# Kernel tuning notes

Hardware: AMD Instinct MI355X
Metric: run time of the kernel (lower is better)

## Reference

```python
import jax, jax.numpy as jnp
import numpy as np

B, T, EMB, NDIM = 8, 2048, 1024, 1024


def setup_inputs() -> dict:
    key = jax.random.key(0)
    k1, k2, k3, k4 = jax.random.split(key, 4)
    X = jax.random.normal(k1, (B, T, EMB), dtype=jnp.float32)
    # Linear(emb, ndim, bias=False); stored as [emb, ndim] so projection is X @ W.
    scale = 1.0 / np.sqrt(EMB)
    Wq = jax.random.normal(k2, (EMB, NDIM), dtype=jnp.float32) * scale
    Wk = jax.random.normal(k3, (EMB, NDIM), dtype=jnp.float32) * scale
    Wv = jax.random.normal(k4, (EMB, NDIM), dtype=jnp.float32) * scale
    return {"X": X, "Wq": Wq, "Wk": Wk, "Wv": Wv}


def reference(X, Wq, Wk, Wv):
    ndim = Wq.shape[-1]
    T_ = X.shape[1]
    Q = X @ Wq  # [B,T,ndim]
    K = X @ Wk  # [B,T,ndim]
    V = X @ Wv  # [B,T,ndim]
    # scores[b,t,s] = Q[b,t] . K[b,s], scaled by ndim^-0.5
    scores = jnp.einsum("btd,bsd->bts", Q, K) * (ndim ** -0.5)
    mask = jnp.tril(jnp.ones((T_, T_), dtype=bool))  # causal lower-triangular
    scores = jnp.where(mask, scores, -jnp.inf)
    # NOTE: source uses F.softmax(..., dim=1) -> normalize over the QUERY axis
    # (columns of the [T,T] matrix), not the usual key axis. Replicated faithfully.
    probs = jax.nn.softmax(scores, axis=1)
    # dropout is identity in eval / p=0 deterministic baseline
    return probs @ V  # [B,T,ndim]
```

## Files before the change

kernel.cpp:

```cpp
#include <hip/hip_runtime.h>
#include <hip/hip_bf16.h>

#define B_   8
#define T_   2048
#define EMB_ 1024
#define ND_  1024
#define NTB2 8

typedef __attribute__((ext_vector_type(8))) short   bf8_t;
typedef __attribute__((ext_vector_type(4))) float   f32x4;

__device__ __forceinline__ unsigned short f2bf(float f) {
  union { float f; unsigned int u; } c; c.f = f;
  unsigned int u = c.u;
  unsigned int r = (u + 0x7FFFu + ((u >> 16) & 1u)) >> 16;
  return (unsigned short)r;
}

__device__ __forceinline__ float bf2f(unsigned short b) {
  union { unsigned int u; float f; } c; c.u = ((unsigned int)b) << 16;
  return c.f;
}

__device__ __forceinline__ void gload_lds16(const unsigned short* g, unsigned short* l) {
  __builtin_amdgcn_global_load_lds(
      (const __attribute__((address_space(1))) unsigned int*)g,
      (__attribute__((address_space(3))) unsigned int*)l,
      16, 0, 0);
}

#define SB0() __builtin_amdgcn_sched_barrier(0)
#define BAR() __builtin_amdgcn_s_barrier()

__device__ __forceinline__ void stage_half(const unsigned short* __restrict__ g, int lda,
                                           unsigned short* lhalf, int wave, int lane) {
  const int r3 = lane >> 3, c3 = lane & 7;
  const int colsw = ((c3 ^ r3) << 3);
#pragma unroll
  for (int j = 0; j < 2; ++j) {
    const int row = wave * 8 + r3 + 64 * j;
    gload_lds16(g + (size_t)row * lda + colsw, lhalf + wave * 512 + j * 4096);
  }
}

__device__ __forceinline__ bf8_t read_frag(const unsigned short* half, int r, int ks, int lane) {
  const int col = (((ks) << 5) + ((lane >> 4) << 3)) ^ ((r & 7) << 3);
  return *(const bf8_t*)(half + r * 64 + col);
}

__device__ __forceinline__ int swz_ep(int x) { return ((x >> 1) & 7) << 4; }

__global__ void __launch_bounds__(256) cvt_x_kernel(const float* __restrict__ in,
                                                    unsigned short* __restrict__ out) {
  const int i = (blockIdx.x * 256 + threadIdx.x) * 4;
  float4 v = *(const float4*)(in + i);
  ushort4 o = make_ushort4(f2bf(v.x), f2bf(v.y), f2bf(v.z), f2bf(v.w));
  *(ushort4*)(out + i) = o;
}

__global__ void __launch_bounds__(256) transpose_w_kernel(const float* __restrict__ W,
                                                          unsigned short* __restrict__ Wt,
                                                          float cscale) {
  __shared__ unsigned short tile[32][33];
  const int n0 = blockIdx.x * 32, k0 = blockIdx.y * 32;
  const int tx = threadIdx.x & 31, ty = threadIdx.x >> 5;
#pragma unroll
  for (int r = 0; r < 32; r += 8) {
    float v = W[(size_t)(k0 + ty + r) * ND_ + n0 + tx];
    tile[tx][ty + r] = f2bf(v * cscale);
  }
  __syncthreads();
#pragma unroll
  for (int r = 0; r < 32; r += 8) {
    Wt[(size_t)(n0 + ty + r) * EMB_ + k0 + tx] = tile[ty + r][tx];
  }
}

#define MFMA_QUAD(MB, AF, AOFF) do { \
  __builtin_amdgcn_s_setprio(1); \
  _Pragma("unroll") \
  for (int mi = 0; mi < 2; ++mi) \
    _Pragma("unroll") \
    for (int nf = 0; nf < 4; ++nf) \
      _Pragma("unroll") \
      for (int ks = 0; ks < 2; ++ks) \
        acc[(MB) * 2 + mi][nf] = __builtin_amdgcn_mfma_f32_16x16x32_bf16( \
            (AF)[(AOFF) + mi][ks], bfr[nf][ks], acc[(MB) * 2 + mi][nf], 0, 0, 0); \
  __builtin_amdgcn_s_setprio(0); \
} while (0)

#define MFMA_Q8(MB) do { \
  __builtin_amdgcn_s_setprio(1); \
  _Pragma("unroll") \
  for (int nf = 0; nf < 4; ++nf) \
    _Pragma("unroll") \
    for (int ks = 0; ks < 2; ++ks) \
      acc[(MB)][nf] = __builtin_amdgcn_mfma_f32_16x16x32_bf16( \
          af[(MB)][ks], bfr[nf][ks], acc[(MB)][nf], 0, 0, 0); \
  __builtin_amdgcn_s_setprio(0); \
} while (0)

#define LDSA(d, h) (lds256 + ((d) * 2 + (h)) * 8192)
#define LDSB(d, h) (lds256 + 32768 + ((d) * 2 + (h)) * 8192)

#define GEMM256_LOOP(ABASE, BBASE, LDK) \
  stage_half((ABASE),                             (LDK), LDSA(0, 0), wave, lane); \
  stage_half((ABASE) + (size_t)128 * (LDK),       (LDK), LDSA(0, 1), wave, lane); \
  stage_half((BBASE),                             (LDK), LDSB(0, 0), wave, lane); \
  stage_half((BBASE) + (size_t)128 * (LDK),       (LDK), LDSB(0, 1), wave, lane); \
  stage_half((BBASE) + 64,                        (LDK), LDSB(1, 0), wave, lane); \
  stage_half((BBASE) + (size_t)128 * (LDK) + 64,  (LDK), LDSB(1, 1), wave, lane); \
  stage_half((ABASE) + 64,                        (LDK), LDSA(1, 0), wave, lane); \
  stage_half((ABASE) + (size_t)128 * (LDK) + 64,  (LDK), LDSA(1, 1), wave, lane); \
  asm volatile("s_waitcnt vmcnt(8)" ::: "memory"); \
  SB0(); BAR(); SB0(); \
  for (int t = 0; t < 16; ++t) { \
    const int d = t & 1; \
    const unsigned short* Ah = LDSA(d, wm); \
    const unsigned short* Bh = LDSB(d, wn >> 1); \
    bf8_t bfr[4][2], af[4][2]; \
    _Pragma("unroll") \
    for (int nf = 0; nf < 4; ++nf) \
      _Pragma("unroll") \
      for (int ks = 0; ks < 2; ++ks) bfr[nf][ks] = read_frag(Bh, brow + nf * 16, ks, lane); \
    _Pragma("unroll") \
    for (int mf = 0; mf < 4; ++mf) \
      _Pragma("unroll") \
      for (int ks = 0; ks < 2; ++ks) af[mf][ks] = read_frag(Ah, arow + mf * 16, ks, lane); \
    SB0(); BAR(); SB0(); \
    MFMA_QUAD(0, af, 0); \
    SB0(); \
    asm volatile("s_waitcnt lgkmcnt(0)" ::: "memory"); \
    SB0(); BAR(); SB0(); \
    if (t < 14) { \
      stage_half((BBASE) + (size_t)(t + 2) * 64,                     (LDK), LDSB(d, 0), wave, lane); \
      stage_half((BBASE) + (size_t)128 * (LDK) + (size_t)(t + 2) * 64,(LDK), LDSB(d, 1), wave, lane); \
    } \
    SB0(); BAR(); SB0(); \
    MFMA_QUAD(1, af, 2); \
    SB0(); BAR(); SB0(); \
    bf8_t af2[4][2]; \
    _Pragma("unroll") \
    for (int mf = 0; mf < 4; ++mf) \
      _Pragma("unroll") \
      for (int ks = 0; ks < 2; ++ks) af2[mf][ks] = read_frag(Ah, arow + (mf + 4) * 16, ks, lane); \
    SB0(); BAR(); SB0(); \
    MFMA_QUAD(2, af2, 0); \
    SB0(); \
    asm volatile("s_waitcnt lgkmcnt(0)" ::: "memory"); \
    SB0(); BAR(); SB0(); \
    if (t < 14) { \
      stage_half((ABASE) + (size_t)(t + 2) * 64,                     (LDK), LDSA(d, 0), wave, lane); \
      stage_half((ABASE) + (size_t)128 * (LDK) + (size_t)(t + 2) * 64,(LDK), LDSA(d, 1), wave, lane); \
      asm volatile("s_waitcnt vmcnt(8)" ::: "memory"); \
    } else if (t == 14) { \
      asm volatile("s_waitcnt vmcnt(0)" ::: "memory"); \
    } \
    SB0(); BAR(); SB0(); \
    MFMA_QUAD(3, af2, 2); \
    SB0(); BAR(); SB0(); \
  }

template <int OUTMODE>
__global__ void __launch_bounds__(512, 2)
gemm_xw256_kernel(const unsigned short* __restrict__ A,
                  const unsigned short* __restrict__ Bt,
                  unsigned short* __restrict__ C) {
  extern __shared__ unsigned short lds256[];
  const int tid = threadIdx.x, lane = tid & 63, wave = tid >> 6;
  const int wm = wave >> 2, wn = wave & 3;
  const int m0 = blockIdx.y * 256, n0 = blockIdx.x * 256;
  const unsigned short* Ab = A + (size_t)m0 * EMB_;
  const unsigned short* Bb = Bt + (size_t)n0 * EMB_;
  f32x4 acc[8][4];
#pragma unroll
  for (int i = 0; i < 8; ++i)
#pragma unroll
    for (int j = 0; j < 4; ++j)
#pragma unroll
      for (int q = 0; q < 4; ++q) acc[i][j][q] = 0.f;
  const int arow = lane & 15;
  const int brow = (wn & 1) * 64 + (lane & 15);

  GEMM256_LOOP(Ab, Bb, EMB_)

  const int cc = lane & 15, cr4 = (lane >> 4) << 2;
#pragma unroll
  for (int mf = 0; mf < 8; ++mf)
#pragma unroll
    for (int nf = 0; nf < 4; ++nf)
#pragma unroll
      for (int q = 0; q < 4; ++q) {
        const int r = wm * 128 + mf * 16 + cr4 + q;
        const int c = wn * 64 + nf * 16 + cc;
        const unsigned short bv = f2bf(acc[mf][nf][q]);
        const int byte = (OUTMODE == 1) ? (c * 512 + ((r * 2) ^ swz_ep(c)))
                                        : (r * 512 + ((c * 2) ^ swz_ep(r)));
        lds256[byte >> 1] = bv;
      }
  __syncthreads();
  if (OUTMODE == 0) {
#pragma unroll
    for (int p = 0; p < 16; ++p) {
      const int o = p * 8192 + tid * 16;
      const int ri = o >> 9, cb = o & 511;
      const bf8_t v = *(const bf8_t*)(lds256 + (((o & ~511) | (cb ^ swz_ep(ri))) >> 1));
      *(bf8_t*)(C + (size_t)(m0 + ri) * ND_ + n0 + (cb >> 1)) = v;
    }
  } else {
    const int bb = m0 >> 11, tt0 = m0 & 2047;
#pragma unroll
    for (int p = 0; p < 16; ++p) {
      const int o = p * 8192 + tid * 16;
      const int ci = o >> 9, rb = o & 511;
      const bf8_t v = *(const bf8_t*)(lds256 + (((o & ~511) | (rb ^ swz_ep(ci))) >> 1));
      *(bf8_t*)(C + ((size_t)bb * ND_ + n0 + ci) * T_ + tt0 + (rb >> 1)) = v;
    }
  }
}

__global__ void __launch_bounds__(512, 2)
scoretile576_kernel(const unsigned short* __restrict__ Qb,
                    const unsigned short* __restrict__ Kb,
                    unsigned short* __restrict__ Pp,
                    float* __restrict__ pm) {
  extern __shared__ unsigned short lds256[];
  const int id = blockIdx.x;
  const int b = id & 7;
  const int r = id >> 3;
  int sc = 0, pfx = 0;
#pragma unroll 8
  for (int i = 0; i < 8; ++i) {
    const int cnt = 16 - 2 * sc;
    if (pfx + cnt <= r) { pfx += cnt; ++sc; }
  }
  const int tr = 2 * sc + (r - pfx);
  const int t0 = tr * 128, s0 = sc * 256;
  const int tid = threadIdx.x, lane = tid & 63, wave = tid >> 6;
  const int wm = wave >> 2, wn = wave & 3;
  const int arow = lane & 15;
  const unsigned short* Ab = Qb + ((size_t)b * T_ + t0) * ND_;
  const unsigned short* Bb = Kb + ((size_t)b * T_ + s0) * ND_;
  f32x4 acc[4][4];
#pragma unroll
  for (int i = 0; i < 4; ++i)
#pragma unroll
    for (int j = 0; j < 4; ++j)
#pragma unroll
      for (int q = 0; q < 4; ++q) acc[i][j][q] = 0.f;

  stage_half(Ab,                           ND_, lds256,                     wave, lane);
  stage_half(Bb,                           ND_, lds256 + 16384,             wave, lane);
  stage_half(Bb + (size_t)128 * ND_,       ND_, lds256 + 16384 + 8192,      wave, lane);
  stage_half(Ab + 64,                      ND_, lds256 + 8192,              wave, lane);
  stage_half(Bb + 64,                      ND_, lds256 + 16384 + 2 * 8192,  wave, lane);
  stage_half(Bb + (size_t)128 * ND_ + 64,  ND_, lds256 + 16384 + 3 * 8192,  wave, lane);
  asm volatile("s_waitcnt vmcnt(6)" ::: "memory");
  SB0(); BAR(); SB0();

  for (int t = 0; t < 16; ++t) {
    const int d = t & 1;
    const unsigned short* Ah = lds256 + d * 8192;
    const unsigned short* Bh = lds256 + 16384 + (d * 2 + (wn >> 1)) * 8192;
    bf8_t bfr[4][2], af[4][2];
#pragma unroll
    for (int nf = 0; nf < 4; ++nf)
#pragma unroll
      for (int ks = 0; ks < 2; ++ks)
        bfr[nf][ks] = read_frag(Bh, (wn & 1) * 64 + nf * 16 + arow, ks, lane);
#pragma unroll
    for (int mf = 0; mf < 4; ++mf)
#pragma unroll
      for (int ks = 0; ks < 2; ++ks)
        af[mf][ks] = read_frag(Ah, wm * 64 + mf * 16 + arow, ks, lane);
    SB0(); BAR(); SB0();
    MFMA_Q8(0);
    SB0();
    asm volatile("s_waitcnt lgkmcnt(0)" ::: "memory");
    SB0(); BAR(); SB0();
    if (t < 14) {
      stage_half(Ab + (size_t)(t + 2) * 64, ND_, lds256 + d * 8192, wave, lane);
      stage_half(Bb + (size_t)(t + 2) * 64, ND_, lds256 + 16384 + (d * 2) * 8192, wave, lane);
    }
    SB0(); BAR(); SB0();
    MFMA_Q8(1);
    SB0(); BAR(); SB0();
    if (t < 14)
      stage_half(Bb + (size_t)128 * ND_ + (size_t)(t + 2) * 64, ND_, lds256 + 16384 + (d * 2 + 1) * 8192, wave, lane);
    SB0(); BAR(); SB0();
    MFMA_Q8(2);
    SB0(); BAR(); SB0();
    if (t < 14)      { asm volatile("s_waitcnt vmcnt(6)" ::: "memory"); }
    else if (t == 14){ asm volatile("s_waitcnt vmcnt(0)" ::: "memory"); }
    SB0(); BAR(); SB0();
    MFMA_Q8(3);
    SB0(); BAR(); SB0();
  }

  __syncthreads();
  const int cc = lane & 15, cr4 = (lane >> 4) << 2;
  float csum[4];
#pragma unroll
  for (int nf = 0; nf < 4; ++nf) csum[nf] = 0.f;
#pragma unroll
  for (int mf = 0; mf < 4; ++mf)
#pragma unroll
    for (int nf = 0; nf < 4; ++nf)
#pragma unroll
      for (int q = 0; q < 4; ++q) {
        const int rr = wm * 64 + mf * 16 + cr4 + q;
        const int c  = wn * 64 + nf * 16 + cc;
        const bool ok = (t0 + rr) >= (s0 + c);
        unsigned short bv = 0;
        if (ok) {
          bv = f2bf(__expf(fminf(acc[mf][nf][q], 30.f)));
          csum[nf] += bf2f(bv);
        }
        lds256[(rr * 512 + ((c * 2) ^ swz_ep(rr))) >> 1] = bv;
      }
  __syncthreads();
  unsigned short* Pbase = Pp + (size_t)b * T_ * T_;
#pragma unroll
  for (int p = 0; p < 8; ++p) {
    const int o = p * 8192 + tid * 16;
    const int ri = o >> 9, cb = o & 511;
    const bf8_t v = *(const bf8_t*)(lds256 + (((o & ~511) | (cb ^ swz_ep(ri))) >> 1));
    *(bf8_t*)(Pbase + (size_t)(t0 + ri) * T_ + s0 + (cb >> 1)) = v;
  }
#pragma unroll
  for (int nf = 0; nf < 4; ++nf) {
    csum[nf] += __shfl_xor(csum[nf], 16);
    csum[nf] += __shfl_xor(csum[nf], 32);
  }
  __syncthreads();
  float* red = (float*)lds256;
  if (lane < 16) {
#pragma unroll
    for (int nf = 0; nf < 4; ++nf)
      red[((wm * 4 + wn) * 4 + nf) * 16 + lane] = csum[nf];
  }
  __syncthreads();
  if (wm == 0 && lane < 16) {
    const size_t base = (((size_t)b * 8 + sc) * 16 + tr) * 256;
#pragma unroll
    for (int nf = 0; nf < 4; ++nf) {
      const float s = red[((0 * 4 + wn) * 4 + nf) * 16 + lane] +
                      red[((1 * 4 + wn) * 4 + nf) * 16 + lane];
      pm[base + wn * 64 + nf * 16 + lane] = s;
    }
  }
}

__global__ void __launch_bounds__(256) colreduce_kernel(const float* __restrict__ pm,
                                                        float* __restrict__ colinv) {
  const int sc = blockIdx.x, b = blockIdx.y, c = threadIdx.x;
  float l = 0.f;
  for (int tr = 2 * sc; tr < 16; ++tr)
    l += pm[(((size_t)b * 8 + sc) * 16 + tr) * 256 + c];
  colinv[(size_t)b * T_ + sc * 256 + c] = 1.0f / l;
}

__global__ void __launch_bounds__(256) vscale_kernel(unsigned short* __restrict__ Vt,
                                                     const float* __restrict__ colinv) {
  const int idx = blockIdx.x * 256 + threadIdx.x;
  const int s8 = (idx * 8) & (T_ - 1);
  const int bd = idx / (T_ / 8);
  const int b = bd >> 10;
  unsigned short* p = Vt + (size_t)bd * T_ + s8;
  bf8_t v = *(bf8_t*)p;
#pragma unroll
  for (int j = 0; j < 8; ++j) {
    const float f = bf2f((unsigned short)v[j]) * colinv[(size_t)b * T_ + s8 + j];
    v[j] = (short)f2bf(f);
  }
  *(bf8_t*)p = v;
}

__device__ __forceinline__ void pv_segment(const unsigned short* __restrict__ Ab,
                                           const unsigned short* __restrict__ Bb,
                                           float* __restrict__ Cb,
                                           int ktiles, unsigned short* lds256,
                                           int lane, int wave) {
  const int wm = wave >> 2, wn = wave & 3;
  const int arow = lane & 15;
  f32x4 acc[4][4];
#pragma unroll
  for (int i = 0; i < 4; ++i)
#pragma unroll
    for (int j = 0; j < 4; ++j)
#pragma unroll
      for (int q = 0; q < 4; ++q) acc[i][j][q] = 0.f;

  stage_half(Ab,                           T_, lds256,                     wave, lane);
  stage_half(Bb,                           T_, lds256 + 16384,             wave, lane);
  stage_half(Bb + (size_t)128 * T_,        T_, lds256 + 16384 + 8192,      wave, lane);
  stage_half(Ab + 64,                      T_, lds256 + 8192,              wave, lane);
  stage_half(Bb + 64,                      T_, lds256 + 16384 + 2 * 8192,  wave, lane);
  stage_half(Bb + (size_t)128 * T_ + 64,   T_, lds256 + 16384 + 3 * 8192,  wave, lane);
  asm volatile("s_waitcnt vmcnt(6)" ::: "memory");
  SB0(); BAR(); SB0();

  for (int t = 0; t < ktiles; ++t) {
    const int d = t & 1;
    const unsigned short* Ah = lds256 + d * 8192;
    const unsigned short* Bh = lds256 + 16384 + (d * 2 + (wn >> 1)) * 8192;
    bf8_t bfr[4][2], af[4][2];
#pragma unroll
    for (int nf = 0; nf < 4; ++nf)
#pragma unroll
      for (int ks = 0; ks < 2; ++ks)
        bfr[nf][ks] = read_frag(Bh, (wn & 1) * 64 + nf * 16 + arow, ks, lane);
#pragma unroll
    for (int mf = 0; mf < 4; ++mf)
#pragma unroll
      for (int ks = 0; ks < 2; ++ks)
        af[mf][ks] = read_frag(Ah, wm * 64 + mf * 16 + arow, ks, lane);
    SB0(); BAR(); SB0();
    MFMA_Q8(0);
    SB0();
    asm volatile("s_waitcnt lgkmcnt(0)" ::: "memory");
    SB0(); BAR(); SB0();
    if (t < ktiles - 2) {
      stage_half(Ab + (size_t)(t + 2) * 64, T_, lds256 + d * 8192, wave, lane);
      stage_half(Bb + (size_t)(t + 2) * 64, T_, lds256 + 16384 + (d * 2) * 8192, wave, lane);
    }
    SB0(); BAR(); SB0();
    MFMA_Q8(1);
    SB0(); BAR(); SB0();
    if (t < ktiles - 2)
      stage_half(Bb + (size_t)128 * T_ + (size_t)(t + 2) * 64, T_, lds256 + 16384 + (d * 2 + 1) * 8192, wave, lane);
    SB0(); BAR(); SB0();
    MFMA_Q8(2);
    SB0(); BAR(); SB0();
    if (t < ktiles - 2)      { asm volatile("s_waitcnt vmcnt(6)" ::: "memory"); }
    else if (t == ktiles - 2){ asm volatile("s_waitcnt vmcnt(0)" ::: "memory"); }
    SB0(); BAR(); SB0();
    MFMA_Q8(3);
    SB0(); BAR(); SB0();
  }

  const int cc = lane & 15, cr4 = (lane >> 4) << 2;
#pragma unroll
  for (int mf = 0; mf < 4; ++mf)
#pragma unroll
    for (int nf = 0; nf < 4; ++nf)
#pragma unroll
      for (int q = 0; q < 4; ++q) {
        const int row = wm * 64 + mf * 16 + cr4 + q;
        const int col = wn * 64 + nf * 16 + cc;
        Cb[(size_t)row * ND_ + col] = acc[mf][nf][q];
      }
}

__global__ void __launch_bounds__(512, 2)
gemm_pv256_kernel(const unsigned short* __restrict__ Pb,
                  const unsigned short* __restrict__ Vt,
                  float* __restrict__ out) {
  extern __shared__ unsigned short lds256[];
  const int b = blockIdx.x & 7;
  const int pair = (blockIdx.x >> 3) & 7;
  const int ncol = blockIdx.x >> 6;
  const int tid = threadIdx.x, lane = tid & 63, wave = tid >> 6;
  const int tbs[2] = {pair, 15 - pair};
#pragma unroll
  for (int si = 0; si < 2; ++si) {
    const int tb = tbs[si];
    const int ktiles = 2 * tb + 2;
    pv_segment(Pb + (size_t)b * T_ * T_ + (size_t)tb * 128 * T_,
               Vt + (size_t)b * ND_ * T_ + (size_t)ncol * 256 * T_,
               out + (size_t)b * T_ * ND_ + (size_t)tb * 128 * ND_ + ncol * 256,
               ktiles, lds256, lane, wave);
  }
}

extern "C" void kernel_launch(void* const* d_in, const int* in_sizes, int n_in,
                              void* d_out, int out_size, void* d_ws, size_t ws_size,
                              hipStream_t stream) {
  const float* X  = (const float*)d_in[0];
  const float* Wq = (const float*)d_in[1];
  const float* Wk = (const float*)d_in[2];
  const float* Wv = (const float*)d_in[3];
  float* out = (float*)d_out;
  (void)in_sizes; (void)n_in; (void)out_size;

  char* ws = (char*)d_ws;
  size_t off = 0;
  auto alloc = [&](size_t bytes) {
    void* p = ws + off;
    off += (bytes + 255) & ~(size_t)255;
    return p;
  };
  unsigned short* Xb  = (unsigned short*)alloc((size_t)B_ * T_ * EMB_ * 2);
  unsigned short* Wtq = (unsigned short*)alloc((size_t)ND_ * EMB_ * 2);
  unsigned short* Wtk = (unsigned short*)alloc((size_t)ND_ * EMB_ * 2);
  unsigned short* Wtv = (unsigned short*)alloc((size_t)ND_ * EMB_ * 2);
  unsigned short* Qb  = (unsigned short*)alloc((size_t)B_ * T_ * ND_ * 2);
  unsigned short* Kb  = (unsigned short*)alloc((size_t)B_ * T_ * ND_ * 2);
  unsigned short* Vt  = (unsigned short*)alloc((size_t)B_ * ND_ * T_ * 2);
  float* colinv = (float*)alloc((size_t)B_ * T_ * 4);
  float* pm     = (float*)alloc((size_t)B_ * 8 * 16 * 256 * 4);
  unsigned short* Pb  = (unsigned short*)alloc((size_t)B_ * T_ * T_ * 2);
  if (off > ws_size) return;

  hipFuncSetAttribute((const void*)&gemm_xw256_kernel<0>,
                      hipFuncAttributeMaxDynamicSharedMemorySize, 131072);
  hipFuncSetAttribute((const void*)&gemm_xw256_kernel<1>,
                      hipFuncAttributeMaxDynamicSharedMemorySize, 131072);
  hipFuncSetAttribute((const void*)&scoretile576_kernel,
                      hipFuncAttributeMaxDynamicSharedMemorySize, 98304);
  hipFuncSetAttribute((const void*)&gemm_pv256_kernel,
                      hipFuncAttributeMaxDynamicSharedMemorySize, 98304);

  hipLaunchKernelGGL(cvt_x_kernel, dim3((B_ * T_ * EMB_) / 1024), dim3(256), 0, stream, X, Xb);
  hipLaunchKernelGGL(transpose_w_kernel, dim3(32, 32), dim3(256), 0, stream, Wq, Wtq, 0.03125f);
  hipLaunchKernelGGL(transpose_w_kernel, dim3(32, 32), dim3(256), 0, stream, Wk, Wtk, 1.0f);
  hipLaunchKernelGGL(transpose_w_kernel, dim3(32, 32), dim3(256), 0, stream, Wv, Wtv, 1.0f);
  hipLaunchKernelGGL((gemm_xw256_kernel<0>), dim3(ND_ / 256, (B_ * T_) / 256), dim3(512), 131072, stream, Xb, Wtq, Qb);
  hipLaunchKernelGGL((gemm_xw256_kernel<0>), dim3(ND_ / 256, (B_ * T_) / 256), dim3(512), 131072, stream, Xb, Wtk, Kb);
  hipLaunchKernelGGL((gemm_xw256_kernel<1>), dim3(ND_ / 256, (B_ * T_) / 256), dim3(512), 131072, stream, Xb, Wtv, Vt);
  hipLaunchKernelGGL(scoretile576_kernel, dim3(576), dim3(512), 98304, stream, Qb, Kb, Pb, pm);
  hipLaunchKernelGGL(colreduce_kernel, dim3(8, B_), dim3(256), 0, stream, pm, colinv);
  hipLaunchKernelGGL(vscale_kernel, dim3((B_ * ND_ * T_) / 8 / 256), dim3(256), 0, stream, Vt, colinv);
  hipLaunchKernelGGL(gemm_pv256_kernel, dim3(NTB2 * 4 * B_), dim3(512), 98304, stream, Pb, Vt, out);
}
```

Baseline: 284.9 us.

## Fuse QKV projections into one launch and use 256x256 triangular score tiles

The three X·W projection GEMMs become one 768-block launch over a concatenated transposed weight buffer. Block IDs are remapped so each XCD works on a contiguous group of M rows, which should improve L2 reuse of X. The score kernel moves from 128x256 tiles (576 blocks) to 256x256 tiles (288 blocks) decoded from a triangular index, reusing the shared GEMM256 loop; only diagonal tiles apply the causal mask, and the partial column-sum layout and column reduction are adjusted to match. Larger tiles raise arithmetic intensity but give fewer blocks, so the score phase has coarser load balance across CUs.

```diff
diff --git a/kernel.cpp b/kernel.cpp
--- a/kernel.cpp
+++ b/kernel.cpp
@@ -27,6 +27,14 @@
       (const __attribute__((address_space(1))) unsigned int*)g,
       (__attribute__((address_space(3))) unsigned int*)l,
       16, 0, 0);
+}
+
+__device__ __forceinline__ void tri_decode(int p, int& tblk, int& sblk) {
+  int t = (int)((sqrtf(8.0f * (float)p + 1.0f) - 1.0f) * 0.5f);
+  while ((t + 1) * (t + 2) / 2 <= p) ++t;
+  while (t * (t + 1) / 2 > p) --t;
+  tblk = t;
+  sblk = p - t * (t + 1) / 2;
 }
 
 #define SB0() __builtin_amdgcn_sched_barrier(0)
@@ -161,30 +169,37 @@
     SB0(); BAR(); SB0(); \
   }
 
-template <int OUTMODE>
 __global__ void __launch_bounds__(512, 2)
-gemm_xw256_kernel(const unsigned short* __restrict__ A,
-                  const unsigned short* __restrict__ Bt,
-                  unsigned short* __restrict__ C) {
+gemm_qkv_kernel(const unsigned short* __restrict__ A,
+                const unsigned short* __restrict__ Wt3,
+                unsigned short* __restrict__ Qb,
+                unsigned short* __restrict__ Kb,
+                unsigned short* __restrict__ Vt) {
   extern __shared__ unsigned short lds256[];
+  const int id = blockIdx.x;
+  const int xcd = id & 7, j = id >> 3;
+  const int nIdx = j >> 3;
+  const int mloc = j & 7;
+  const int m0 = (xcd * 8 + mloc) * 256;
+  const int n0 = nIdx * 256;
   const int tid = threadIdx.x, lane = tid & 63, wave = tid >> 6;
   const int wm = wave >> 2, wn = wave & 3;
-  const int m0 = blockIdx.y * 256, n0 = blockIdx.x * 256;
   const unsigned short* Ab = A + (size_t)m0 * EMB_;
-  const unsigned short* Bb = Bt + (size_t)n0 * EMB_;
+  const unsigned short* Bb = Wt3 + (size_t)n0 * EMB_;
   f32x4 acc[8][4];
 #pragma unroll
   for (int i = 0; i < 8; ++i)
 #pragma unroll
-    for (int j = 0; j < 4; ++j)
-#pragma unroll
-      for (int q = 0; q < 4; ++q) acc[i][j][q] = 0.f;
+    for (int jj = 0; jj < 4; ++jj)
+#pragma unroll
+      for (int q = 0; q < 4; ++q) acc[i][jj][q] = 0.f;
   const int arow = lane & 15;
   const int brow = (wn & 1) * 64 + (lane & 15);
 
   GEMM256_LOOP(Ab, Bb, EMB_)
 
   const int cc = lane & 15, cr4 = (lane >> 4) << 2;
+  const bool isV = (nIdx >= 8);
 #pragma unroll
   for (int mf = 0; mf < 8; ++mf)
 #pragma unroll
@@ -194,123 +209,76 @@
         const int r = wm * 128 + mf * 16 + cr4 + q;
         const int c = wn * 64 + nf * 16 + cc;
         const unsigned short bv = f2bf(acc[mf][nf][q]);
-        const int byte = (OUTMODE == 1) ? (c * 512 + ((r * 2) ^ swz_ep(c)))
-                                        : (r * 512 + ((c * 2) ^ swz_ep(r)));
+        const int byte = isV ? (c * 512 + ((r * 2) ^ swz_ep(c)))
+                             : (r * 512 + ((c * 2) ^ swz_ep(r)));
         lds256[byte >> 1] = bv;
       }
   __syncthreads();
-  if (OUTMODE == 0) {
+  if (!isV) {
+    unsigned short* C = (nIdx < 4) ? Qb : Kb;
+    const int colbase = (nIdx < 4) ? n0 : (n0 - 1024);
 #pragma unroll
     for (int p = 0; p < 16; ++p) {
       const int o = p * 8192 + tid * 16;
       const int ri = o >> 9, cb = o & 511;
       const bf8_t v = *(const bf8_t*)(lds256 + (((o & ~511) | (cb ^ swz_ep(ri))) >> 1));
-      *(bf8_t*)(C + (size_t)(m0 + ri) * ND_ + n0 + (cb >> 1)) = v;
+      *(bf8_t*)(C + (size_t)(m0 + ri) * ND_ + colbase + (cb >> 1)) = v;
     }
   } else {
+    const int colbase = n0 - 2048;
     const int bb = m0 >> 11, tt0 = m0 & 2047;
 #pragma unroll
     for (int p = 0; p < 16; ++p) {
       const int o = p * 8192 + tid * 16;
       const int ci = o >> 9, rb = o & 511;
       const bf8_t v = *(const bf8_t*)(lds256 + (((o & ~511) | (rb ^ swz_ep(ci))) >> 1));
-      *(bf8_t*)(C + ((size_t)bb * ND_ + n0 + ci) * T_ + tt0 + (rb >> 1)) = v;
+      *(bf8_t*)(Vt + ((size_t)bb * ND_ + colbase + ci) * T_ + tt0 + (rb >> 1)) = v;
     }
   }
 }
 
 __global__ void __launch_bounds__(512, 2)
-scoretile576_kernel(const unsigned short* __restrict__ Qb,
+scoretile288_kernel(const unsigned short* __restrict__ Qb,
                     const unsigned short* __restrict__ Kb,
                     unsigned short* __restrict__ Pp,
                     float* __restrict__ pm) {
   extern __shared__ unsigned short lds256[];
   const int id = blockIdx.x;
   const int b = id & 7;
-  const int r = id >> 3;
-  int sc = 0, pfx = 0;
-#pragma unroll 8
-  for (int i = 0; i < 8; ++i) {
-    const int cnt = 16 - 2 * sc;
-    if (pfx + cnt <= r) { pfx += cnt; ++sc; }
-  }
-  const int tr = 2 * sc + (r - pfx);
-  const int t0 = tr * 128, s0 = sc * 256;
+  int tr, sr;
+  tri_decode(id >> 3, tr, sr);
+  const int t0 = tr * 256, s0 = sr * 256;
   const int tid = threadIdx.x, lane = tid & 63, wave = tid >> 6;
   const int wm = wave >> 2, wn = wave & 3;
-  const int arow = lane & 15;
   const unsigned short* Ab = Qb + ((size_t)b * T_ + t0) * ND_;
   const unsigned short* Bb = Kb + ((size_t)b * T_ + s0) * ND_;
-  f32x4 acc[4][4];
-#pragma unroll
-  for (int i = 0; i < 4; ++i)
-#pragma unroll
-    for (int j = 0; j < 4; ++j)
-#pragma unroll
-      for (int q = 0; q < 4; ++q) acc[i][j][q] = 0.f;
-
-  stage_half(Ab,                           ND_, lds256,                     wave, lane);
-  stage_half(Bb,                           ND_, lds256 + 16384,             wave, lane);
-  stage_half(Bb + (size_t)128 * ND_,       ND_, lds256 + 16384 + 8192,      wave, lane);
-  stage_half(Ab + 64,                      ND_, lds256 + 8192,              wave, lane);
-  stage_half(Bb + 64,                      ND_, lds256 + 16384 + 2 * 8192,  wave, lane);
-  stage_half(Bb + (size_t)128 * ND_ + 64,  ND_, lds256 + 16384 + 3 * 8192,  wave, lane);
-  asm volatile("s_waitcnt vmcnt(6)" ::: "memory");
-  SB0(); BAR(); SB0();
-
-  for (int t = 0; t < 16; ++t) {
-    const int d = t & 1;
-    const unsigned short* Ah = lds256 + d * 8192;
-    const unsigned short* Bh = lds256 + 16384 + (d * 2 + (wn >> 1)) * 8192;
-    bf8_t bfr[4][2], af[4][2];
+  f32x4 acc[8][4];
+#pragma unroll
+  for (int i = 0; i < 8; ++i)
+#pragma unroll
+    for (int jj = 0; jj < 4; ++jj)
+#pragma unroll
+      for (int q = 0; q < 4; ++q) acc[i][jj][q] = 0.f;
+  const int arow = lane & 15;
+  const int brow = (wn & 1) * 64 + (lane & 15);
+
+  GEMM256_LOOP(Ab, Bb, ND_)
+
+  __syncthreads();
+  const int cc = lane & 15, cr4 = (lane >> 4) << 2;
+  const bool diag = (tr == sr);
+  float csum[4];
+#pragma unroll
+  for (int nf = 0; nf < 4; ++nf) csum[nf] = 0.f;
+#pragma unroll
+  for (int mf = 0; mf < 8; ++mf)
 #pragma unroll
     for (int nf = 0; nf < 4; ++nf)
 #pragma unroll
-      for (int ks = 0; ks < 2; ++ks)
-        bfr[nf][ks] = read_frag(Bh, (wn & 1) * 64 + nf * 16 + arow, ks, lane);
-#pragma unroll
-    for (int mf = 0; mf < 4; ++mf)
-#pragma unroll
-      for (int ks = 0; ks < 2; ++ks)
-        af[mf][ks] = read_frag(Ah, wm * 64 + mf * 16 + arow, ks, lane);
-    SB0(); BAR(); SB0();
-    MFMA_Q8(0);
-    SB0();
-    asm volatile("s_waitcnt lgkmcnt(0)" ::: "memory");
-    SB0(); BAR(); SB0();
-    if (t < 14) {
-      stage_half(Ab + (size_t)(t + 2) * 64, ND_, lds256 + d * 8192, wave, lane);
-      stage_half(Bb + (size_t)(t + 2) * 64, ND_, lds256 + 16384 + (d * 2) * 8192, wave, lane);
-    }
-    SB0(); BAR(); SB0();
-    MFMA_Q8(1);
-    SB0(); BAR(); SB0();
-    if (t < 14)
-      stage_half(Bb + (size_t)128 * ND_ + (size_t)(t + 2) * 64, ND_, lds256 + 16384 + (d * 2 + 1) * 8192, wave, lane);
-    SB0(); BAR(); SB0();
-    MFMA_Q8(2);
-    SB0(); BAR(); SB0();
-    if (t < 14)      { asm volatile("s_waitcnt vmcnt(6)" ::: "memory"); }
-    else if (t == 14){ asm volatile("s_waitcnt vmcnt(0)" ::: "memory"); }
-    SB0(); BAR(); SB0();
-    MFMA_Q8(3);
-    SB0(); BAR(); SB0();
-  }
-
-  __syncthreads();
-  const int cc = lane & 15, cr4 = (lane >> 4) << 2;
-  float csum[4];
-#pragma unroll
-  for (int nf = 0; nf < 4; ++nf) csum[nf] = 0.f;
-#pragma unroll
-  for (int mf = 0; mf < 4; ++mf)
-#pragma unroll
-    for (int nf = 0; nf < 4; ++nf)
-#pragma unroll
       for (int q = 0; q < 4; ++q) {
-        const int rr = wm * 64 + mf * 16 + cr4 + q;
+        const int rr = wm * 128 + mf * 16 + cr4 + q;
         const int c  = wn * 64 + nf * 16 + cc;
-        const bool ok = (t0 + rr) >= (s0 + c);
+        const bool ok = !diag || ((t0 + rr) >= (s0 + c));
         unsigned short bv = 0;
         if (ok) {
           bv = f2bf(__expf(fminf(acc[mf][nf][q], 30.f)));
@@ -321,7 +289,7 @@
   __syncthreads();
   unsigned short* Pbase = Pp + (size_t)b * T_ * T_;
 #pragma unroll
-  for (int p = 0; p < 8; ++p) {
+  for (int p = 0; p < 16; ++p) {
     const int o = p * 8192 + tid * 16;
     const int ri = o >> 9, cb = o & 511;
     const bf8_t v = *(const bf8_t*)(lds256 + (((o & ~511) | (cb ^ swz_ep(ri))) >> 1));
@@ -341,7 +309,7 @@
   }
   __syncthreads();
   if (wm == 0 && lane < 16) {
-    const size_t base = (((size_t)b * 8 + sc) * 16 + tr) * 256;
+    const size_t base = (((size_t)b * 8 + sr) * 8 + tr) * 256;
 #pragma unroll
     for (int nf = 0; nf < 4; ++nf) {
       const float s = red[((0 * 4 + wn) * 4 + nf) * 16 + lane] +
@@ -355,8 +323,8 @@
                                                         float* __restrict__ colinv) {
   const int sc = blockIdx.x, b = blockIdx.y, c = threadIdx.x;
   float l = 0.f;
-  for (int tr = 2 * sc; tr < 16; ++tr)
-    l += pm[(((size_t)b * 8 + sc) * 16 + tr) * 256 + c];
+  for (int tr = sc; tr < 8; ++tr)
+    l += pm[(((size_t)b * 8 + sc) * 8 + tr) * 256 + c];
   colinv[(size_t)b * T_ + sc * 256 + c] = 1.0f / l;
 }
 
@@ -491,34 +459,32 @@
     return p;
   };
   unsigned short* Xb  = (unsigned short*)alloc((size_t)B_ * T_ * EMB_ * 2);
-  unsigned short* Wtq = (unsigned short*)alloc((size_t)ND_ * EMB_ * 2);
-  unsigned short* Wtk = (unsigned short*)alloc((size_t)ND_ * EMB_ * 2);
-  unsigned short* Wtv = (unsigned short*)alloc((size_t)ND_ * EMB_ * 2);
+  unsigned short* Wt3 = (unsigned short*)alloc((size_t)3 * ND_ * EMB_ * 2);
   unsigned short* Qb  = (unsigned short*)alloc((size_t)B_ * T_ * ND_ * 2);
   unsigned short* Kb  = (unsigned short*)alloc((size_t)B_ * T_ * ND_ * 2);
   unsigned short* Vt  = (unsigned short*)alloc((size_t)B_ * ND_ * T_ * 2);
   float* colinv = (float*)alloc((size_t)B_ * T_ * 4);
-  float* pm     = (float*)alloc((size_t)B_ * 8 * 16 * 256 * 4);
+  float* pm     = (float*)alloc((size_t)B_ * 8 * 8 * 256 * 4);
   unsigned short* Pb  = (unsigned short*)alloc((size_t)B_ * T_ * T_ * 2);
   if (off > ws_size) return;
 
-  hipFuncSetAttribute((const void*)&gemm_xw256_kernel<0>,
+  hipFuncSetAttribute((const void*)&gemm_qkv_kernel,
                       hipFuncAttributeMaxDynamicSharedMemorySize, 131072);
-  hipFuncSetAttribute((const void*)&gemm_xw256_kernel<1>,
+  hipFuncSetAttribute((const void*)&scoretile288_kernel,
                       hipFuncAttributeMaxDynamicSharedMemorySize, 131072);
-  hipFuncSetAttribute((const void*)&scoretile576_kernel,
-                      hipFuncAttributeMaxDynamicSharedMemorySize, 98304);
   hipFuncSetAttribute((const void*)&gemm_pv256_kernel,
                       hipFuncAttributeMaxDynamicSharedMemorySize, 98304);
 
   hipLaunchKernelGGL(cvt_x_kernel, dim3((B_ * T_ * EMB_) / 1024), dim3(256), 0, stream, X, Xb);
-  hipLaunchKernelGGL(transpose_w_kernel, dim3(32, 32), dim3(256), 0, stream, Wq, Wtq, 0.03125f);
-  hipLaunchKernelGGL(transpose_w_kernel, dim3(32, 32), dim3(256), 0, stream, Wk, Wtk, 1.0f);
-  hipLaunchKernelGGL(transpose_w_kernel, dim3(32, 32), dim3(256), 0, stream, Wv, Wtv, 1.0f);
-  hipLaunchKernelGGL((gemm_xw256_kernel<0>), dim3(ND_ / 256, (B_ * T_) / 256), dim3(512), 131072, stream, Xb, Wtq, Qb);
-  hipLaunchKernelGGL((gemm_xw256_kernel<0>), dim3(ND_ / 256, (B_ * T_) / 256), dim3(512), 131072, stream, Xb, Wtk, Kb);
-  hipLaunchKernelGGL((gemm_xw256_kernel<1>), dim3(ND_ / 256, (B_ * T_) / 256), dim3(512), 131072, stream, Xb, Wtv, Vt);
-  hipLaunchKernelGGL(scoretile576_kernel, dim3(576), dim3(512), 98304, stream, Qb, Kb, Pb, pm);
+  hipLaunchKernelGGL(transpose_w_kernel, dim3(32, 32), dim3(256), 0, stream,
+                     Wq, Wt3, 0.03125f);
+  hipLaunchKernelGGL(transpose_w_kernel, dim3(32, 32), dim3(256), 0, stream,
+                     Wk, Wt3 + (size_t)ND_ * EMB_, 1.0f);
+  hipLaunchKernelGGL(transpose_w_kernel, dim3(32, 32), dim3(256), 0, stream,
+                     Wv, Wt3 + (size_t)2 * ND_ * EMB_, 1.0f);
+  hipLaunchKernelGGL(gemm_qkv_kernel, dim3(768), dim3(512), 131072, stream,
+                     Xb, Wt3, Qb, Kb, Vt);
+  hipLaunchKernelGGL(scoretile288_kernel, dim3(288), dim3(512), 131072, stream, Qb, Kb, Pb, pm);
   hipLaunchKernelGGL(colreduce_kernel, dim3(8, B_), dim3(256), 0, stream, pm, colinv);
   hipLaunchKernelGGL(vscale_kernel, dim3((B_ * ND_ * T_) / 8 / 256), dim3(256), 0, stream, Vt, colinv);
   hipLaunchKernelGGL(gemm_pv256_kernel, dim3(NTB2 * 4 * B_), dim3(512), 98304, stream, Pb, Vt, out);
```

Measured after the change: 293.2 us. +2.9%, slower.

## Merge QKV projections and use 256x256 score tiles with mixed tail

Applied to the files above, without the earlier changes.

Fuses the three weight transposes and three projection GEMMs into single launches indexed by blockIdx.z. Reworks the score kernel so 256 blocks compute 256x256 triangular tiles, found by decoding a triangular index, and 64 extra blocks compute 128x256 half-tiles for the last row band on columns 4-7 to balance load. The partial column-sum layout and the reduction kernel are updated to match. The goal is fewer launches, more reuse per tile and better balance across CUs, at the cost of more LDS per block and fewer total blocks in the score stage.

```diff
diff --git a/kernel.cpp b/kernel.cpp
--- a/kernel.cpp
+++ b/kernel.cpp
@@ -27,6 +27,14 @@
       (const __attribute__((address_space(1))) unsigned int*)g,
       (__attribute__((address_space(3))) unsigned int*)l,
       16, 0, 0);
+}
+
+__device__ __forceinline__ void tri_decode(int p, int& tblk, int& sblk) {
+  int t = (int)((sqrtf(8.0f * (float)p + 1.0f) - 1.0f) * 0.5f);
+  while ((t + 1) * (t + 2) / 2 <= p) ++t;
+  while (t * (t + 1) / 2 > p) --t;
+  tblk = t;
+  sblk = p - t * (t + 1) / 2;
 }
 
 #define SB0() __builtin_amdgcn_sched_barrier(0)
@@ -58,10 +66,15 @@
   *(ushort4*)(out + i) = o;
 }
 
-__global__ void __launch_bounds__(256) transpose_w_kernel(const float* __restrict__ W,
-                                                          unsigned short* __restrict__ Wt,
-                                                          float cscale) {
+__global__ void __launch_bounds__(256) transpose_w3_kernel(const float* __restrict__ Wq,
+                                                           const float* __restrict__ Wk,
+                                                           const float* __restrict__ Wv,
+                                                           unsigned short* __restrict__ Wt3) {
   __shared__ unsigned short tile[32][33];
+  const int z = blockIdx.z;
+  const float* W = (z == 0) ? Wq : (z == 1) ? Wk : Wv;
+  const float cscale = (z == 0) ? 0.03125f : 1.0f;
+  unsigned short* Wt = Wt3 + (size_t)z * ND_ * EMB_;
   const int n0 = blockIdx.x * 32, k0 = blockIdx.y * 32;
   const int tx = threadIdx.x & 31, ty = threadIdx.x >> 5;
 #pragma unroll
@@ -161,12 +174,15 @@
     SB0(); BAR(); SB0(); \
   }
 
-template <int OUTMODE>
 __global__ void __launch_bounds__(512, 2)
-gemm_xw256_kernel(const unsigned short* __restrict__ A,
-                  const unsigned short* __restrict__ Bt,
-                  unsigned short* __restrict__ C) {
+gemm_xw3_kernel(const unsigned short* __restrict__ A,
+                const unsigned short* __restrict__ Wt3,
+                unsigned short* __restrict__ Qb,
+                unsigned short* __restrict__ Kb,
+                unsigned short* __restrict__ Vt) {
   extern __shared__ unsigned short lds256[];
+  const int z = blockIdx.z;
+  const unsigned short* Bt = Wt3 + (size_t)z * ND_ * EMB_;
   const int tid = threadIdx.x, lane = tid & 63, wave = tid >> 6;
   const int wm = wave >> 2, wn = wave & 3;
   const int m0 = blockIdx.y * 256, n0 = blockIdx.x * 256;
@@ -185,6 +201,7 @@
   GEMM256_LOOP(Ab, Bb, EMB_)
 
   const int cc = lane & 15, cr4 = (lane >> 4) << 2;
+  const bool isV = (z == 2);
 #pragma unroll
   for (int mf = 0; mf < 8; ++mf)
 #pragma unroll
@@ -194,12 +211,13 @@
         const int r = wm * 128 + mf * 16 + cr4 + q;
         const int c = wn * 64 + nf * 16 + cc;
         const unsigned short bv = f2bf(acc[mf][nf][q]);
-        const int byte = (OUTMODE == 1) ? (c * 512 + ((r * 2) ^ swz_ep(c)))
-                                        : (r * 512 + ((c * 2) ^ swz_ep(r)));
+        const int byte = isV ? (c * 512 + ((r * 2) ^ swz_ep(c)))
+                             : (r * 512 + ((c * 2) ^ swz_ep(r)));
         lds256[byte >> 1] = bv;
       }
   __syncthreads();
-  if (OUTMODE == 0) {
+  if (!isV) {
+    unsigned short* C = (z == 0) ? Qb : Kb;
 #pragma unroll
     for (int p = 0; p < 16; ++p) {
       const int o = p * 8192 + tid * 16;
@@ -214,139 +232,208 @@
       const int o = p * 8192 + tid * 16;
       const int ci = o >> 9, rb = o & 511;
       const bf8_t v = *(const bf8_t*)(lds256 + (((o & ~511) | (rb ^ swz_ep(ci))) >> 1));
-      *(bf8_t*)(C + ((size_t)bb * ND_ + n0 + ci) * T_ + tt0 + (rb >> 1)) = v;
+      *(bf8_t*)(Vt + ((size_t)bb * ND_ + n0 + ci) * T_ + tt0 + (rb >> 1)) = v;
     }
   }
 }
 
 __global__ void __launch_bounds__(512, 2)
-scoretile576_kernel(const unsigned short* __restrict__ Qb,
-                    const unsigned short* __restrict__ Kb,
-                    unsigned short* __restrict__ Pp,
-                    float* __restrict__ pm) {
+scoretile_mixed_kernel(const unsigned short* __restrict__ Qb,
+                       const unsigned short* __restrict__ Kb,
+                       unsigned short* __restrict__ Pp,
+                       float* __restrict__ pm) {
   extern __shared__ unsigned short lds256[];
   const int id = blockIdx.x;
-  const int b = id & 7;
-  const int r = id >> 3;
-  int sc = 0, pfx = 0;
-#pragma unroll 8
-  for (int i = 0; i < 8; ++i) {
-    const int cnt = 16 - 2 * sc;
-    if (pfx + cnt <= r) { pfx += cnt; ++sc; }
-  }
-  const int tr = 2 * sc + (r - pfx);
-  const int t0 = tr * 128, s0 = sc * 256;
   const int tid = threadIdx.x, lane = tid & 63, wave = tid >> 6;
   const int wm = wave >> 2, wn = wave & 3;
   const int arow = lane & 15;
-  const unsigned short* Ab = Qb + ((size_t)b * T_ + t0) * ND_;
-  const unsigned short* Bb = Kb + ((size_t)b * T_ + s0) * ND_;
-  f32x4 acc[4][4];
-#pragma unroll
-  for (int i = 0; i < 4; ++i)
-#pragma unroll
-    for (int j = 0; j < 4; ++j)
-#pragma unroll
-      for (int q = 0; q < 4; ++q) acc[i][j][q] = 0.f;
-
-  stage_half(Ab,                           ND_, lds256,                     wave, lane);
-  stage_half(Bb,                           ND_, lds256 + 16384,             wave, lane);
-  stage_half(Bb + (size_t)128 * ND_,       ND_, lds256 + 16384 + 8192,      wave, lane);
-  stage_half(Ab + 64,                      ND_, lds256 + 8192,              wave, lane);
-  stage_half(Bb + 64,                      ND_, lds256 + 16384 + 2 * 8192,  wave, lane);
-  stage_half(Bb + (size_t)128 * ND_ + 64,  ND_, lds256 + 16384 + 3 * 8192,  wave, lane);
-  asm volatile("s_waitcnt vmcnt(6)" ::: "memory");
-  SB0(); BAR(); SB0();
-
-  for (int t = 0; t < 16; ++t) {
-    const int d = t & 1;
-    const unsigned short* Ah = lds256 + d * 8192;
-    const unsigned short* Bh = lds256 + 16384 + (d * 2 + (wn >> 1)) * 8192;
-    bf8_t bfr[4][2], af[4][2];
-#pragma unroll
-    for (int nf = 0; nf < 4; ++nf)
-#pragma unroll
-      for (int ks = 0; ks < 2; ++ks)
-        bfr[nf][ks] = read_frag(Bh, (wn & 1) * 64 + nf * 16 + arow, ks, lane);
+  const int cc = lane & 15, cr4 = (lane >> 4) << 2;
+
+  if (id < 256) {
+    const int b = id & 7;
+    int tr, sr;
+    tri_decode(id >> 3, tr, sr);
+    const int t0 = tr * 256, s0 = sr * 256;
+    const unsigned short* Ab = Qb + ((size_t)b * T_ + t0) * ND_;
+    const unsigned short* Bb = Kb + ((size_t)b * T_ + s0) * ND_;
+    f32x4 acc[8][4];
+#pragma unroll
+    for (int i = 0; i < 8; ++i)
+#pragma unroll
+      for (int jj = 0; jj < 4; ++jj)
+#pragma unroll
+        for (int q = 0; q < 4; ++q) acc[i][jj][q] = 0.f;
+    const int brow = (wn & 1) * 64 + (lane & 15);
+
+    GEMM256_LOOP(Ab, Bb, ND_)
+
+    __syncthreads();
+    const bool diag = (tr == sr);
+    float csum[4];
+#pragma unroll
+    for (int nf = 0; nf < 4; ++nf) csum[nf] = 0.f;
+#pragma unroll
+    for (int mf = 0; mf < 8; ++mf)
+#pragma unroll
+      for (int nf = 0; nf < 4; ++nf)
+#pragma unroll
+        for (int q = 0; q < 4; ++q) {
+          const int rr = wm * 128 + mf * 16 + cr4 + q;
+          const int c  = wn * 64 + nf * 16 + cc;
+          const bool ok = !diag || ((t0 + rr) >= (s0 + c));
+          unsigned short bv = 0;
+          if (ok) {
+            bv = f2bf(__expf(fminf(acc[mf][nf][q], 30.f)));
+            csum[nf] += bf2f(bv);
+          }
+          lds256[(rr * 512 + ((c * 2) ^ swz_ep(rr))) >> 1] = bv;
+        }
+    __syncthreads();
+    unsigned short* Pbase = Pp + (size_t)b * T_ * T_;
+#pragma unroll
+    for (int p = 0; p < 16; ++p) {
+      const int o = p * 8192 + tid * 16;
+      const int ri = o >> 9, cb = o & 511;
+      const bf8_t v = *(const bf8_t*)(lds256 + (((o & ~511) | (cb ^ swz_ep(ri))) >> 1));
+      *(bf8_t*)(Pbase + (size_t)(t0 + ri) * T_ + s0 + (cb >> 1)) = v;
+    }
+#pragma unroll
+    for (int nf = 0; nf < 4; ++nf) {
+      csum[nf] += __shfl_xor(csum[nf], 16);
+      csum[nf] += __shfl_xor(csum[nf], 32);
+    }
+    __syncthreads();
+    float* red = (float*)lds256;
+    if (lane < 16) {
+#pragma unroll
+      for (int nf = 0; nf < 4; ++nf)
+        red[((wm * 4 + wn) * 4 + nf) * 16 + lane] = csum[nf];
+    }
+    __syncthreads();
+    if (wm == 0 && lane < 16) {
+      const size_t base = (((size_t)b * 8 + sr) * 10 + tr) * 256;
+#pragma unroll
+      for (int nf = 0; nf < 4; ++nf) {
+        const float s = red[((0 * 4 + wn) * 4 + nf) * 16 + lane] +
+                        red[((1 * 4 + wn) * 4 + nf) * 16 + lane];
+        pm[base + wn * 64 + nf * 16 + lane] = s;
+      }
+    }
+  } else {
+    const int fid = id - 256;
+    const int b = fid & 7;
+    const int f = fid >> 3;
+    const int sr = 4 + (f >> 1);
+    const int half = f & 1;
+    const int t0 = 7 * 256 + half * 128, s0 = sr * 256;
+    const unsigned short* Ab = Qb + ((size_t)b * T_ + t0) * ND_;
+    const unsigned short* Bb = Kb + ((size_t)b * T_ + s0) * ND_;
+    f32x4 acc[4][4];
+#pragma unroll
+    for (int i = 0; i < 4; ++i)
+#pragma unroll
+      for (int jj = 0; jj < 4; ++jj)
+#pragma unroll
+        for (int q = 0; q < 4; ++q) acc[i][jj][q] = 0.f;
+
+    stage_half(Ab,                           ND_, lds256,                     wave, lane);
+    stage_half(Bb,                           ND_, lds256 + 16384,             wave, lane);
+    stage_half(Bb + (size_t)128 * ND_,       ND_, lds256 + 16384 + 8192,      wave, lane);
+    stage_half(Ab + 64,                      ND_, lds256 + 8192,              wave, lane);
+    stage_half(Bb + 64,                      ND_, lds256 + 16384 + 2 * 8192,  wave, lane);
+    stage_half(Bb + (size_t)128 * ND_ + 64,  ND_, lds256 + 16384 + 3 * 8192,  wave, lane);
+    asm volatile("s_waitcnt vmcnt(6)" ::: "memory");
+    SB0(); BAR(); SB0();
+
+    for (int t = 0; t < 16; ++t) {
+      const int d = t & 1;
+      const unsigned short* Ah = lds256 + d * 8192;
+      const unsigned short* Bh = lds256 + 16384 + (d * 2 + (wn >> 1)) * 8192;
+      bf8_t bfr[4][2], af[4][2];
+#pragma unroll
+      for (int nf = 0; nf < 4; ++nf)
+#pragma unroll
+        for (int ks = 0; ks < 2; ++ks)
+          bfr[nf][ks] = read_frag(Bh, (wn & 1) * 64 + nf * 16 + arow, ks, lane);
+#pragma unroll
+      for (int mf = 0; mf < 4; ++mf)
+#pragma unroll
+        for (int ks = 0; ks < 2; ++ks)
+          af[mf][ks] = read_frag(Ah, wm * 64 + mf * 16 + arow, ks, lane);
+      SB0(); BAR(); SB0();
+      MFMA_Q8(0);
+      SB0();
+      asm volatile("s_waitcnt lgkmcnt(0)" ::: "memory");
+      SB0(); BAR(); SB0();
+      if (t < 14) {
+        stage_half(Ab + (size_t)(t + 2) * 64, ND_, lds256 + d * 8192, wave, lane);
+        stage_half(Bb + (size_t)(t + 2) * 64, ND_, lds256 + 16384 + (d * 2) * 8192, wave, lane);
+      }
+      SB0(); BAR(); SB0();
+      MFMA_Q8(1);
+      SB0(); BAR(); SB0();
+      if (t < 14)
+        stage_half(Bb + (size_t)128 * ND_ + (size_t)(t + 2) * 64, ND_, lds256 + 16384 + (d * 2 + 1) * 8192, wave, lane);
+      SB0(); BAR(); SB0();
+      MFMA_Q8(2);
+      SB0(); BAR(); SB0();
+      if (t < 14)      { asm volatile("s_waitcnt vmcnt(6)" ::: "memory"); }
+      else if (t == 14){ asm volatile("s_waitcnt vmcnt(0)" ::: "memory"); }
+      SB0(); BAR(); SB0();
+      MFMA_Q8(3);
+      SB0(); BAR(); SB0();
+    }
+
+    __syncthreads();
+    float csum[4];
+#pragma unroll
+    for (int nf = 0; nf < 4; ++nf) csum[nf] = 0.f;
 #pragma unroll
     for (int mf = 0; mf < 4; ++mf)
 #pragma unroll
-      for (int ks = 0; ks < 2; ++ks)
-        af[mf][ks] = read_frag(Ah, wm * 64 + mf * 16 + arow, ks, lane);
-    SB0(); BAR(); SB0();
-    MFMA_Q8(0);
-    SB0();
-    asm volatile("s_waitcnt lgkmcnt(0)" ::: "memory");
-    SB0(); BAR(); SB0();
-    if (t < 14) {
-      stage_half(Ab + (size_t)(t + 2) * 64, ND_, lds256 + d * 8192, wave, lane);
-      stage_half(Bb + (size_t)(t + 2) * 64, ND_, lds256 + 16384 + (d * 2) * 8192, wave, lane);
-    }
-    SB0(); BAR(); SB0();
-    MFMA_Q8(1);
-    SB0(); BAR(); SB0();
-    if (t < 14)
-      stage_half(Bb + (size_t)128 * ND_ + (size_t)(t + 2) * 64, ND_, lds256 + 16384 + (d * 2 + 1) * 8192, wave, lane);
-    SB0(); BAR(); SB0();
-    MFMA_Q8(2);
-    SB0(); BAR(); SB0();
-    if (t < 14)      { asm volatile("s_waitcnt vmcnt(6)" ::: "memory"); }
-    else if (t == 14){ asm volatile("s_waitcnt vmcnt(0)" ::: "memory"); }
-    SB0(); BAR(); SB0();
-    MFMA_Q8(3);
-    SB0(); BAR(); SB0();
-  }
-
-  __syncthreads();
-  const int cc = lane & 15, cr4 = (lane >> 4) << 2;
-  float csum[4];
-#pragma unroll
-  for (int nf = 0; nf < 4; ++nf) csum[nf] = 0.f;
-#pragma unroll
-  for (int mf = 0; mf < 4; ++mf)
-#pragma unroll
-    for (int nf = 0; nf < 4; ++nf)
-#pragma unroll
-      for (int q = 0; q < 4; ++q) {
-        const int rr = wm * 64 + mf * 16 + cr4 + q;
-        const int c  = wn * 64 + nf * 16 + cc;
-        const bool ok = (t0 + rr) >= (s0 + c);
-        unsigned short bv = 0;
-        if (ok) {
-          bv = f2bf(__expf(fminf(acc[mf][nf][q], 30.f)));
-          csum[nf] += bf2f(bv);
+      for (int nf = 0; nf < 4; ++nf)
+#pragma unroll
+        for (int q = 0; q < 4; ++q) {
+          const int rr = wm * 64 + mf * 16 + cr4 + q;
+          const int c  = wn * 64 + nf * 16 + cc;
+          const bool ok = (t0 + rr) >= (s0 + c);
+          unsigned short bv = 0;
+          if (ok) {
+            bv = f2bf(__expf(fminf(acc[mf][nf][q], 30.f)));
+            csum[nf] += bf2f(bv);
+          }
+          lds256[(rr * 512 + ((c * 2) ^ swz_ep(rr))) >> 1] = bv;
         }
-        lds256[(rr * 512 + ((c * 2) ^ swz_ep(rr))) >> 1] = bv;
+    __syncthreads();
+    unsigned short* Pbase = Pp + (size_t)b * T_ * T_;
+#pragma unroll
+    for (int p = 0; p < 8; ++p) {
+      const int o = p * 8192 + tid * 16;
+      const int ri = o >> 9, cb = o & 511;
+      const bf8_t v = *(const bf8_t*)(lds256 + (((o & ~511) | (cb ^ swz_ep(ri))) >> 1));
+      *(bf8_t*)(Pbase + (size_t)(t0 + ri) * T_ + s0 + (cb >> 1)) = v;
+    }
+#pragma unroll
+    for (int nf = 0; nf < 4; ++nf) {
+      csum[nf] += __shfl_xor(csum[nf], 16);
+      csum[nf] += __shfl_xor(csum[nf], 32);
+    }
+    __syncthreads();
+    float* red = (float*)lds256;
+    if (lane < 16) {
+#pragma unroll
+      for (int nf = 0; nf < 4; ++nf)
+        red[((wm * 4 + wn) * 4 + nf) * 16 + lane] = csum[nf];
+    }
+    __syncthreads();
+    if (wm == 0 && lane < 16) {
+      const size_t base = (((size_t)b * 8 + sr) * 10 + 8 + half) * 256;
+#pragma unroll
+      for (int nf = 0; nf < 4; ++nf) {
+        const float s = red[((0 * 4 + wn) * 4 + nf) * 16 + lane] +
+                        red[((1 * 4 + wn) * 4 + nf) * 16 + lane];
+        pm[base + wn * 64 + nf * 16 + lane] = s;
       }
-  __syncthreads();
-  unsigned short* Pbase = Pp + (size_t)b * T_ * T_;
-#pragma unroll
-  for (int p = 0; p < 8; ++p) {
-    const int o = p * 8192 + tid * 16;
-    const int ri = o >> 9, cb = o & 511;
-    const bf8_t v = *(const bf8_t*)(lds256 + (((o & ~511) | (cb ^ swz_ep(ri))) >> 1));
-    *(bf8_t*)(Pbase + (size_t)(t0 + ri) * T_ + s0 + (cb >> 1)) = v;
-  }
-#pragma unroll
-  for (int nf = 0; nf < 4; ++nf) {
-    csum[nf] += __shfl_xor(csum[nf], 16);
-    csum[nf] += __shfl_xor(csum[nf], 32);
-  }
-  __syncthreads();
-  float* red = (float*)lds256;
-  if (lane < 16) {
-#pragma unroll
-    for (int nf = 0; nf < 4; ++nf)
-      red[((wm * 4 + wn) * 4 + nf) * 16 + lane] = csum[nf];
-  }
-  __syncthreads();
-  if (wm == 0 && lane < 16) {
-    const size_t base = (((size_t)b * 8 + sc) * 16 + tr) * 256;
-#pragma unroll
-    for (int nf = 0; nf < 4; ++nf) {
-      const float s = red[((0 * 4 + wn) * 4 + nf) * 16 + lane] +
-                      red[((1 * 4 + wn) * 4 + nf) * 16 + lane];
-      pm[base + wn * 64 + nf * 16 + lane] = s;
     }
   }
 }
@@ -355,8 +442,14 @@
                                                         float* __restrict__ colinv) {
   const int sc = blockIdx.x, b = blockIdx.y, c = threadIdx.x;
   float l = 0.f;
-  for (int tr = 2 * sc; tr < 16; ++tr)
-    l += pm[(((size_t)b * 8 + sc) * 16 + tr) * 256 + c];
+  for (int tr = sc; tr < 8; ++tr) {
+    if (sc >= 4 && tr == 7) continue;
+    l += pm[(((size_t)b * 8 + sc) * 10 + tr) * 256 + c];
+  }
+  if (sc >= 4) {
+    l += pm[(((size_t)b * 8 + sc) * 10 + 8) * 256 + c];
+    l += pm[(((size_t)b * 8 + sc) * 10 + 9) * 256 + c];
+  }
   colinv[(size_t)b * T_ + sc * 256 + c] = 1.0f / l;
 }
 
@@ -491,34 +584,27 @@
     return p;
   };
   unsigned short* Xb  = (unsigned short*)alloc((size_t)B_ * T_ * EMB_ * 2);
-  unsigned short* Wtq = (unsigned short*)alloc((size_t)ND_ * EMB_ * 2);
-  unsigned short* Wtk = (unsigned short*)alloc((size_t)ND_ * EMB_ * 2);
-  unsigned short* Wtv = (unsigned short*)alloc((size_t)ND_ * EMB_ * 2);
+  unsigned short* Wt3 = (unsigned short*)alloc((size_t)3 * ND_ * EMB_ * 2);
   unsigned short* Qb  = (unsigned short*)alloc((size_t)B_ * T_ * ND_ * 2);
   unsigned short* Kb  = (unsigned short*)alloc((size_t)B_ * T_ * ND_ * 2);
   unsigned short* Vt  = (unsigned short*)alloc((size_t)B_ * ND_ * T_ * 2);
   float* colinv = (float*)alloc((size_t)B_ * T_ * 4);
-  float* pm     = (float*)alloc((size_t)B_ * 8 * 16 * 256 * 4);
+  float* pm     = (float*)alloc((size_t)B_ * 8 * 10 * 256 * 4);
   unsigned short* Pb  = (unsigned short*)alloc((size_t)B_ * T_ * T_ * 2);
   if (off > ws_size) return;
 
-  hipFuncSetAttribute((const void*)&gemm_xw256_kernel<0>,
+  hipFuncSetAttribute((const void*)&gemm_xw3_kernel,
                       hipFuncAttributeMaxDynamicSharedMemorySize, 131072);
-  hipFuncSetAttribute((const void*)&gemm_xw256_kernel<1>,
+  hipFuncSetAttribute((const void*)&scoretile_mixed_kernel,
                       hipFuncAttributeMaxDynamicSharedMemorySize, 131072);
-  hipFuncSetAttribute((const void*)&scoretile576_kernel,
-                      hipFuncAttributeMaxDynamicSharedMemorySize, 98304);
   hipFuncSetAttribute((const void*)&gemm_pv256_kernel,
                       hipFuncAttributeMaxDynamicSharedMemorySize, 98304);
 
   hipLaunchKernelGGL(cvt_x_kernel, dim3((B_ * T_ * EMB_) / 1024), dim3(256), 0, stream, X, Xb);
-  hipLaunchKernelGGL(transpose_w_kernel, dim3(32, 32), dim3(256), 0, stream, Wq, Wtq, 0.03125f);
-  hipLaunchKernelGGL(transpose_w_kernel, dim3(32, 32), dim3(256), 0, stream, Wk, Wtk, 1.0f);
-  hipLaunchKernelGGL(transpose_w_kernel, dim3(32, 32), dim3(256), 0, stream, Wv, Wtv, 1.0f);
-  hipLaunchKernelGGL((gemm_xw256_kernel<0>), dim3(ND_ / 256, (B_ * T_) / 256), dim3(512), 131072, stream, Xb, Wtq, Qb);
-  hipLaunchKernelGGL((gemm_xw256_kernel<0>), dim3(ND_ / 256, (B_ * T_) / 256), dim3(512), 131072, stream, Xb, Wtk, Kb);
-  hipLaunchKernelGGL((gemm_xw256_kernel<1>), dim3(ND_ / 256, (B_ * T_) / 256), dim3(512), 131072, stream, Xb, Wtv, Vt);
-  hipLaunchKernelGGL(scoretile576_kernel, dim3(576), dim3(512), 98304, stream, Qb, Kb, Pb, pm);
+  hipLaunchKernelGGL(transpose_w3_kernel, dim3(32, 32, 3), dim3(256), 0, stream, Wq, Wk, Wv, Wt3);
+  hipLaunchKernelGGL(gemm_xw3_kernel, dim3(ND_ / 256, (B_ * T_) / 256, 3), dim3(512), 131072, stream,
+                     Xb, Wt3, Qb, Kb, Vt);
+  hipLaunchKernelGGL(scoretile_mixed_kernel, dim3(320), dim3(512), 131072, stream, Qb, Kb, Pb, pm);
   hipLaunchKernelGGL(colreduce_kernel, dim3(8, B_), dim3(256), 0, stream, pm, colinv);
   hipLaunchKernelGGL(vscale_kernel, dim3((B_ * ND_ * T_) / 8 / 256), dim3(256), 0, stream, Vt, colinv);
   hipLaunchKernelGGL(gemm_pv256_kernel, dim3(NTB2 * 4 * B_), dim3(512), 98304, stream, Pb, Vt, out);
```

After: 278.7 us. 1.02x faster.
